# Kernel tuning notes

Hardware: AMD Instinct MI355X
Metric: run time of the kernel (lower is better)

## Reference

```python
import jax, jax.numpy as jnp
import numpy as np

B, T, C = 2, 2048, 2048
H, D = 16, 128


def _rope(x, cos, sin):
    # x: [B,H,T,D], cos/sin: [T,D//2]
    half = x.shape[-1] // 2
    x1, x2 = x[..., :half], x[..., half:]
    c = cos[None, None, :, :]
    s = sin[None, None, :, :]
    return jnp.concatenate([x1 * c - x2 * s, x1 * s + x2 * c], axis=-1)


def setup_inputs() -> dict:
    key = jax.random.key(0)
    k1, k2, k3, k4, k5 = jax.random.split(key, 5)
    x = jax.random.normal(k1, (B, T, C), dtype=jnp.float32)
    cos = jax.random.uniform(k2, (T, D // 2), dtype=jnp.float32)
    sin = jax.random.uniform(k3, (T, D // 2), dtype=jnp.float32)
    scale = 1.0 / np.sqrt(C)
    W_qkv = jax.random.normal(k4, (C, 3 * C), dtype=jnp.float32) * scale
    W_proj = jax.random.normal(k5, (C, C), dtype=jnp.float32) * scale
    return {"x": x, "cos": cos, "sin": sin, "W_qkv": W_qkv, "W_proj": W_proj}


def reference(x, cos, sin, W_qkv, W_proj):
    Bx, Tx, Cx = x.shape
    qkv = x @ W_qkv  # [B,T,3C]
    q, k, v = jnp.split(qkv, 3, axis=-1)
    # [B,T,C] -> [B,H,T,D]
    q = q.reshape(Bx, Tx, H, D).transpose(0, 2, 1, 3)
    k = k.reshape(Bx, Tx, H, D).transpose(0, 2, 1, 3)
    v = v.reshape(Bx, Tx, H, D).transpose(0, 2, 1, 3)
    q = _rope(q, cos, sin)
    k = _rope(k, cos, sin)
    # causal SDPA
    scores = jnp.einsum("bhqd,bhkd->bhqk", q, k) / jnp.sqrt(jnp.float32(D))
    causal = jnp.tril(jnp.ones((Tx, Tx), dtype=bool))
    scores = jnp.where(causal[None, None], scores, jnp.finfo(scores.dtype).min)
    attn = jax.nn.softmax(scores, axis=-1)
    out = jnp.einsum("bhqk,bhkd->bhqd", attn, v)
    out = out.transpose(0, 2, 1, 3).reshape(Bx, Tx, Cx)
    return out @ W_proj
```

## Files before the change

### kernel.cpp

```cpp
#include <hip/hip_runtime.h>
#include <stdint.h>

#define B_  2
#define T_  2048
#define C_  2048
#define H_  16
#define D_  128
#define BH_ 32
#define M_  4096

typedef __attribute__((ext_vector_type(8))) __bf16  bf16x8;
typedef __attribute__((ext_vector_type(4))) float   floatx4;
typedef __attribute__((ext_vector_type(4))) ushort  ushortx4;
typedef __attribute__((ext_vector_type(8))) ushort  ushortx8;

__device__ __forceinline__ ushort f2bf(float f) {
    union { float f; uint32_t u; } v; v.f = f;
    return (ushort)((v.u + 0x7fffu + ((v.u >> 16) & 1u)) >> 16);
}

__device__ __forceinline__ float bf2f(ushort u) {
    union { uint32_t u; float f; } v; v.u = ((uint32_t)u) << 16;
    return v.f;
}

__device__ __forceinline__ floatx4 mfma_bf16(bf16x8 a, bf16x8 b, floatx4 c) {
    return __builtin_amdgcn_mfma_f32_16x16x32_bf16(a, b, c, 0, 0, 0);
}

__device__ __forceinline__ void async16(const ushort* g, ushort* l) {
    __builtin_amdgcn_global_load_lds(
        (const __attribute__((address_space(1))) uint32_t*)g,
        (__attribute__((address_space(3))) uint32_t*)l, 16, 0, 0);
}

__global__ __launch_bounds__(256) void convert_bf16(
    const float* __restrict__ X, ushort* __restrict__ Xb)
{
    const int i = blockIdx.x * 256 + threadIdx.x;
    const float4 v = ((const float4*)X)[i];
    ushortx4 p = { f2bf(v.x), f2bf(v.y), f2bf(v.z), f2bf(v.w) };
    ((ushortx4*)Xb)[i] = p;
}

__global__ __launch_bounds__(256) void transpose_w(
    const float* __restrict__ W, ushort* __restrict__ Wt, int Kdim, int Ndim)
{
    __shared__ float tile[32][33];
    const int n0 = blockIdx.x * 32, k0 = blockIdx.y * 32;
    const int tx = threadIdx.x, ty = threadIdx.y;
    #pragma unroll
    for (int j = 0; j < 4; j++)
        tile[ty + j*8][tx] = W[(size_t)(k0 + ty + j*8) * Ndim + n0 + tx];
    __syncthreads();
    #pragma unroll
    for (int j = 0; j < 4; j++)
        Wt[(size_t)(n0 + ty + j*8) * Kdim + k0 + tx] = f2bf(tile[tx][ty + j*8]);
}

struct FragA { bf16x8 f[4][2]; };
struct FragB { bf16x8 f[2][2]; };

__device__ __forceinline__ void load_a(FragA& fa, const ushort* Ab, int base,
                                       int lr, int quad)
{
    #pragma unroll
    for (int mi2 = 0; mi2 < 4; mi2++)
        #pragma unroll
        for (int kk = 0; kk < 2; kk++) {
            const int row = base + mi2 * 16 + lr;
            fa.f[mi2][kk] = *(const bf16x8*)(
                Ab + row * 64 + (((kk * 4 + quad) ^ (lr & 7)) << 3));
        }
}

__device__ __forceinline__ void load_b(FragB& fb, const ushort* Bb, int base,
                                       int lr, int quad)
{
    #pragma unroll
    for (int ni2 = 0; ni2 < 2; ni2++)
        #pragma unroll
        for (int kk = 0; kk < 2; kk++) {
            const int row = base + ni2 * 16 + lr;
            fb.f[ni2][kk] = *(const bf16x8*)(
                Bb + row * 64 + (((kk * 4 + quad) ^ (lr & 7)) << 3));
        }
}

__device__ __forceinline__ void mfma_quad(floatx4 (&acc)[8][4], const FragA& fa,
                                          const FragB& fb, int mh, int nh)
{
    #pragma unroll
    for (int mi2 = 0; mi2 < 4; mi2++)
        #pragma unroll
        for (int ni2 = 0; ni2 < 2; ni2++)
            #pragma unroll
            for (int kk = 0; kk < 2; kk++)
                acc[mh*4 + mi2][nh*2 + ni2] =
                    mfma_bf16(fa.f[mi2][kk], fb.f[ni2][kk],
                              acc[mh*4 + mi2][nh*2 + ni2]);
}

__device__ __forceinline__ void stage64(const ushort* __restrict__ gsrc,
                                        ushort* ldst, int blk, int k0, int tid)
{
    const int lane = tid & 63;
    const int w8   = tid >> 6;
    const int rl   = lane >> 3;
    const int u    = lane & 7;
    const int row  = (blk << 6) + (w8 << 3) + rl;
    const ushort* g = gsrc + (size_t)row * C_ + k0 + ((u ^ rl) << 3);
    async16(g, ldst + (blk << 12) + (w8 << 9));
}

__device__ __forceinline__ void kloop_8ph(
    const ushort* __restrict__ Ablk, const ushort* __restrict__ Bblk,
    ushort* lds, floatx4 (&acc)[8][4], int tid)
{
    const int lane = tid & 63;
    const int w    = tid >> 6;
    const int wr   = w >> 2;
    const int wc   = w & 3;
    const int lr   = lane & 15;
    const int quad = lane >> 4;

    #pragma unroll
    for (int blk = 0; blk < 4; blk++) {
        stage64(Ablk, lds,         blk, 0, tid);
        stage64(Bblk, lds + 32768, blk, 0, tid);
    }
    #pragma unroll
    for (int blk = 0; blk < 4; blk++) {
        stage64(Ablk, lds + 16384, blk, 64, tid);
        stage64(Bblk, lds + 49152, blk, 64, tid);
    }
    asm volatile("s_waitcnt vmcnt(8)" ::: "memory");
    __builtin_amdgcn_sched_barrier(0);
    __builtin_amdgcn_s_barrier();

    FragA fa0, fa1;
    FragB fb0, fb1;

    #pragma unroll 2
    for (int t = 0; t < 32; ++t) {
        const int p = t & 1;
        ushort* Ab = lds + (p << 14);
        ushort* Bb = lds + 32768 + (p << 14);
        const int k2 = (t + 2) << 6;
        const bool st = (t < 30);

        load_a(fa0, Ab, wr * 128, lr, quad);
        load_b(fb0, Bb, wc * 64, lr, quad);
        __builtin_amdgcn_s_barrier();
        asm volatile("s_waitcnt lgkmcnt(0)" ::: "memory");
        __builtin_amdgcn_sched_barrier(0);
        __builtin_amdgcn_s_setprio(1);
        mfma_quad(acc, fa0, fb0, 0, 0);
        __builtin_amdgcn_s_setprio(0);
        __builtin_amdgcn_s_barrier();

        load_b(fb1, Bb, wc * 64 + 32, lr, quad);
        if (st) { stage64(Ablk, Ab, 0, k2, tid);
                  stage64(Ablk, Ab, 2, k2, tid); }
        __builtin_amdgcn_s_barrier();
        asm volatile("s_waitcnt lgkmcnt(0)" ::: "memory");
        __builtin_amdgcn_sched_barrier(0);
        __builtin_amdgcn_s_setprio(1);
        mfma_quad(acc, fa0, fb1, 0, 1);
        __builtin_amdgcn_s_setprio(0);
        __builtin_amdgcn_s_barrier();

        load_a(fa1, Ab, wr * 128 + 64, lr, quad);
        if (st) { stage64(Bblk, Bb, 0, k2, tid);
                  stage64(Bblk, Bb, 1, k2, tid);
                  stage64(Bblk, Bb, 2, k2, tid); }
        __builtin_amdgcn_s_barrier();
        asm volatile("s_waitcnt lgkmcnt(0)" ::: "memory");
        __builtin_amdgcn_sched_barrier(0);
        __builtin_amdgcn_s_setprio(1);
        mfma_quad(acc, fa1, fb0, 1, 0);
        __builtin_amdgcn_s_setprio(0);
        __builtin_amdgcn_s_barrier();

        if (st) { stage64(Bblk, Bb, 3, k2, tid);
                  stage64(Ablk, Ab, 1, k2, tid);
                  stage64(Ablk, Ab, 3, k2, tid); }
        if (st) asm volatile("s_waitcnt vmcnt(8)" ::: "memory");
        else    asm volatile("s_waitcnt vmcnt(0)" ::: "memory");
        __builtin_amdgcn_sched_barrier(0);
        __builtin_amdgcn_s_barrier();
        __builtin_amdgcn_s_setprio(1);
        mfma_quad(acc, fa1, fb1, 1, 1);
        __builtin_amdgcn_s_setprio(0);
        __builtin_amdgcn_s_barrier();
    }
}

__global__ __launch_bounds__(512, 2) void gemm_bt_8ph(
    const ushort* __restrict__ A, const ushort* __restrict__ Bt,
    float* __restrict__ Co)
{
    __shared__ __align__(16) ushort lds[65536];

    const int tid  = threadIdx.x;
    const int lane = tid & 63;
    const int w    = tid >> 6;
    const int wr   = w >> 2;
    const int wc   = w & 3;
    const int lr   = lane & 15;
    const int quad = lane >> 4;

    int bid = (int)blockIdx.x;
    bid = (bid & 7) * 16 + (bid >> 3);
    const int bx = bid & 7;
    const int by = bid >> 3;

    const ushort* Ablk = A  + (size_t)(by * 256) * C_;
    const ushort* Bblk = Bt + (size_t)(bx * 256) * C_;

    floatx4 acc[8][4];
    #pragma unroll
    for (int i = 0; i < 8; i++)
        #pragma unroll
        for (int j = 0; j < 4; j++)
            acc[i][j] = (floatx4){0.f, 0.f, 0.f, 0.f};

    kloop_8ph(Ablk, Bblk, lds, acc, tid);

    const size_t row0 = (size_t)by * 256 + wr * 128;
    const size_t col0 = (size_t)bx * 256 + wc * 64;
    #pragma unroll
    for (int mi = 0; mi < 8; mi++)
        #pragma unroll
        for (int ni = 0; ni < 4; ni++)
            #pragma unroll
            for (int r = 0; r < 4; r++)
                Co[(row0 + mi*16 + quad*4 + r) * (size_t)C_ + col0 + ni*16 + lr]
                    = acc[mi][ni][r];
}

__global__ __launch_bounds__(512, 2) void gemm_qkv_8ph(
    const ushort* __restrict__ A, const ushort* __restrict__ Bt,
    const float* __restrict__ cosb, const float* __restrict__ sinb,
    ushort* __restrict__ qb, ushort* __restrict__ kbf, ushort* __restrict__ vt)
{
    __shared__ __align__(16) ushort lds[65536];

    const int tid  = threadIdx.x;
    const int lane = tid & 63;
    const int w    = tid >> 6;
    const int wr   = w >> 2;
    const int wc   = w & 3;
    const int lr   = lane & 15;
    const int quad = lane >> 4;

    int bid = (int)blockIdx.x;
    bid = (bid & 7) * 48 + (bid >> 3);
    const int bx = bid % 24;
    const int by = bid / 24;

    const ushort* Ablk = A  + (size_t)(by * 256) * C_;
    const ushort* Bblk = Bt + (size_t)(bx * 256) * C_;

    floatx4 acc[8][4];
    #pragma unroll
    for (int i = 0; i < 8; i++)
        #pragma unroll
        for (int j = 0; j < 4; j++)
            acc[i][j] = (floatx4){0.f, 0.f, 0.f, 0.f};

    kloop_8ph(Ablk, Bblk, lds, acc, tid);

    const int qt  = bx >> 3;
    const int h0  = (bx & 7) << 1;
    const int b   = by >> 3;
    const int t0g = (by & 7) << 8;

    __syncthreads();

    if (qt < 2) {
        #pragma unroll
        for (int mi = 0; mi < 8; mi++)
            #pragma unroll
            for (int ni = 0; ni < 4; ni++)
                #pragma unroll
                for (int r = 0; r < 4; r++) {
                    const int tt = wr * 128 + mi * 16 + quad * 4 + r;
                    const int cc = wc * 64 + ni * 16 + lr;
                    lds[tt * 256 + ((((cc >> 3) ^ (tt & 31)) << 3) | (cc & 7))]
                        = f2bf(acc[mi][ni][r]);
                }
        __syncthreads();

        const int trow = tid >> 1;
        const int hsel = tid & 1;
        const int tg   = t0g + trow;
        const int bh   = b * 16 + h0 + hsel;
        ushort* outp = (qt == 0 ? qb : kbf) + ((size_t)bh * T_ + tg) * D_;
        const float4* cp4 = (const float4*)(cosb + (size_t)tg * 64);
        const float4* sp4 = (const float4*)(sinb + (size_t)tg * 64);
        const ushort* rowp = lds + trow * 256;
        const int tw = trow & 31;
        #pragma unroll
        for (int u = 0; u < 8; u++) {
            bf16x8 x1 = *(const bf16x8*)(rowp + (((hsel * 16 + u)     ^ tw) << 3));
            bf16x8 x2 = *(const bf16x8*)(rowp + (((hsel * 16 + 8 + u) ^ tw) << 3));
            float cc[8], ss[8];
            *(float4*)(cc)     = cp4[u * 2];
            *(float4*)(cc + 4) = cp4[u * 2 + 1];
            *(float4*)(ss)     = sp4[u * 2];
            *(float4*)(ss + 4) = sp4[u * 2 + 1];
            ushortx8 lo, hi;
            #pragma unroll
            for (int e = 0; e < 8; e++) {
                const float x1f = (float)x1[e];
                const float x2f = (float)x2[e];
                lo[e] = f2bf(x1f * cc[e] - x2f * ss[e]);
                hi[e] = f2bf(x1f * ss[e] + x2f * cc[e]);
            }
            *(ushortx8*)(outp + u * 8)      = lo;
            *(ushortx8*)(outp + 64 + u * 8) = hi;
        }
    } else {
        #pragma unroll
        for (int mi = 0; mi < 8; mi++)
            #pragma unroll
            for (int ni = 0; ni < 4; ni++)
                #pragma unroll
                for (int r = 0; r < 4; r++) {
                    const int tt = wr * 128 + mi * 16 + quad * 4 + r;
                    const int cc = wc * 64 + ni * 16 + lr;
                    lds[cc * 256 + ((((tt >> 3) ^ (cc & 31)) << 3) | (tt & 7))]
                        = f2bf(acc[mi][ni][r]);
                }
        __syncthreads();

        const int c  = tid >> 1;
        const int hT = tid & 1;
        const int hh = c >> 7;
        const int d  = c & 127;
        const int bh = b * 16 + h0 + hh;
        const ushort* rowp = lds + c * 256;
        const int cw = c & 31;
        ushort* outp = vt + ((size_t)bh * D_ + d) * T_ + t0g + hT * 128;
        #pragma unroll
        for (int u = 0; u < 16; u++) {
            bf16x8 vv = *(const bf16x8*)(rowp + (((hT * 16 + u) ^ cw) << 3));
            *(bf16x8*)(outp + u * 8) = vv;
        }
    }
}

__global__ __launch_bounds__(256, 4) void flash_attn(
    const ushort* __restrict__ qb, const ushort* __restrict__ kb,
    const ushort* __restrict__ vt, ushort* __restrict__ attnoutb)
{
    __shared__ __align__(16) ushort kt_s[64 * 128];
    __shared__ __align__(16) ushort vt_s[128 * 64];
    __shared__ __align__(16) ushort pl_s[4][16 * 40];

    const int w    = threadIdx.x >> 6;
    const int lane = threadIdx.x & 63;
    const int lr   = lane & 15;
    const int quad = lane >> 4;

    const int bh = blockIdx.x & 31;
    const int m  = 31 - (blockIdx.x >> 5);
    const int qt = 4 * m + w;
    const int qbase = qt * 16;
    const int nk = m + 1;
    const int bb = bh >> 4, hh = bh & 15;

    const ushort* kbp = kb + (size_t)bh * T_ * D_;
    const ushort* vbp = vt + (size_t)bh * D_ * T_;
    ushort* pl = pl_s[w];

    bf16x8 qf[4];
    const ushort* qrow = qb + ((size_t)bh * T_ + qbase + lr) * D_ + quad * 8;
    #pragma unroll
    for (int kc = 0; kc < 4; kc++)
        qf[kc] = *(const bf16x8*)(qrow + kc * 32);

    floatx4 o[8];
    #pragma unroll
    for (int dc = 0; dc < 8; dc++) o[dc] = (floatx4){0.f, 0.f, 0.f, 0.f};
    floatx4 lac = (floatx4){0.f, 0.f, 0.f, 0.f};

    const __bf16 one = (__bf16)1.0f;
    const bf16x8 ones = {one, one, one, one, one, one, one, one};
    const float SCL  = 0.08838834764831845f * 1.4426950408889634f;
    const float BIAS = 23.083120654223414f;

    const int krow4 = lane >> 4;
    const int kunit = lane & 15;
    const int vrow8 = lane >> 3;
    const int vunit = lane & 7;

    for (int kt = 0; kt < nk; ++kt) {
        const int kb0 = kt * 64;
        __syncthreads();
        #pragma unroll
        for (int j = 0; j < 4; j++) {
            const int row = w * 16 + j * 4 + krow4;
            const ushort* gp = kbp + (size_t)(kb0 + row) * D_
                                   + ((kunit ^ (row & 15)) << 3);
            async16(gp, kt_s + (w * 16 + j * 4) * 128);
        }
        #pragma unroll
        for (int j = 0; j < 4; j++) {
            const int row = w * 32 + j * 8 + vrow8;
            const ushort* gp = vbp + (size_t)row * T_ + kb0
                                   + ((vunit ^ (row & 7)) << 3);
            async16(gp, vt_s + (w * 32 + j * 8) * 64);
        }
        __syncthreads();

        #pragma unroll
        for (int half = 0; half < 2; ++half) {
            floatx4 st[2];
            #pragma unroll
            for (int jj = 0; jj < 2; ++jj) {
                const int j = half * 2 + jj;
                floatx4 s = (floatx4){0.f, 0.f, 0.f, 0.f};
                const int kl = j * 16 + lr;
                #pragma unroll
                for (int kc = 0; kc < 4; kc++) {
                    bf16x8 af = *(const bf16x8*)(
                        kt_s + kl * 128 + ((((kc << 2) | quad) ^ lr) << 3));
                    s = mfma_bf16(af, qf[kc], s);
                }
                st[jj] = s;
            }
            #pragma unroll
            for (int jj = 0; jj < 2; ++jj) {
                const int j = half * 2 + jj;
                const int kg0 = kb0 + j * 16 + quad * 4;
                float p[4];
                #pragma unroll
                for (int r = 0; r < 4; r++) {
                    float e = __builtin_amdgcn_exp2f(fmaf(st[jj][r], SCL, -BIAS));
                    p[r] = (kg0 + r > qbase + lr) ? 0.f : e;
                }
                uint2 pk;
                pk.x = (uint32_t)f2bf(p[0]) | ((uint32_t)f2bf(p[1]) << 16);
                pk.y = (uint32_t)f2bf(p[2]) | ((uint32_t)f2bf(p[3]) << 16);
                *(uint2*)(pl + lr * 40 + jj * 16 + quad * 4) = pk;
            }
            bf16x8 pf = *(const bf16x8*)(pl + lr * 40 + quad * 8);
            lac = mfma_bf16(pf, ones, lac);
            #pragma unroll
            for (int dc = 0; dc < 8; dc++) {
                const int d = dc * 16 + lr;
                bf16x8 vf = *(const bf16x8*)(
                    vt_s + d * 64 + ((((half << 2) | quad) ^ (lr & 7)) << 3));
                o[dc] = mfma_bf16(pf, vf, o[dc]);
            }
        }
    }

    #pragma unroll
    for (int dc = 0; dc < 8; dc++)
        #pragma unroll
        for (int r = 0; r < 4; r++) {
            const int trow = qbase + quad * 4 + r;
            attnoutb[((size_t)(bb * T_ + trow)) * C_ + hh * D_ + dc * 16 + lr]
                = f2bf(o[dc][r] / lac[r]);
        }
}

extern "C" void kernel_launch(void* const* d_in, const int* in_sizes, int n_in,
                              void* d_out, int out_size, void* d_ws, size_t ws_size,
                              hipStream_t stream)
{
    (void)in_sizes; (void)n_in; (void)out_size; (void)ws_size;
    const float* x     = (const float*)d_in[0];
    const float* cosb  = (const float*)d_in[1];
    const float* sinb  = (const float*)d_in[2];
    const float* Wqkv  = (const float*)d_in[3];
    const float* Wproj = (const float*)d_in[4];
    float* out = (float*)d_out;

    char* ws = (char*)d_ws;
    ushort* xb       = (ushort*)(ws);
    ushort* Wtq      = (ushort*)(ws + 16777216);
    ushort* Wtp      = (ushort*)(ws + 41943040);
    ushort* qb       = (ushort*)(ws + 50331648);
    ushort* kbf      = (ushort*)(ws + 67108864);
    ushort* vt       = (ushort*)(ws + 83886080);
    ushort* attnoutb = (ushort*)(ws + 100663296);

    dim3 tb32(32, 8);
    transpose_w<<<dim3(3 * C_ / 32, C_ / 32), tb32, 0, stream>>>(Wqkv, Wtq, C_, 3 * C_);
    transpose_w<<<dim3(C_ / 32, C_ / 32),     tb32, 0, stream>>>(Wproj, Wtp, C_, C_);
    convert_bf16<<<(M_ * C_ / 4) / 256, 256, 0, stream>>>(x, xb);

    gemm_qkv_8ph<<<384, 512, 0, stream>>>(xb, Wtq, cosb, sinb, qb, kbf, vt);

    flash_attn<<<BH_ * 32, 256, 0, stream>>>(qb, kbf, vt, attnoutb);

    gemm_bt_8ph<<<128, 512, 0, stream>>>(attnoutb, Wtp, out);
}
```

Before: 412.7 us.

## Replace 8-phase interleaved GEMM k-loop with simpler per-iteration staging schedule

Removes the 8-phase schedule that interleaved global-to-LDS staging with MFMA quads and used barriers between phases. The new loop loads fragments and runs all four MFMA quads with no intermediate barriers, reuses one A fragment register set, then issues all eight staging loads for tile t+2 at the end of the iteration behind a single barrier. This cuts barrier count and register pressure, but global loads are no longer spread across the compute phases, which may reduce overlap of memory and MFMA work.

Result: no change. 416.6 us (+0.9%).

```diff
diff --git a/kernel.cpp b/kernel.cpp
--- a/kernel.cpp
+++ b/kernel.cpp
@@ -113,7 +113,7 @@
     async16(g, ldst + (blk << 12) + (w8 << 9));
 }
 
-__device__ __forceinline__ void kloop_8ph(
+__device__ __forceinline__ void kloop(
     const ushort* __restrict__ Ablk, const ushort* __restrict__ Bblk,
     ushort* lds, floatx4 (&acc)[8][4], int tid)
 {
@@ -138,9 +138,6 @@
     __builtin_amdgcn_sched_barrier(0);
     __builtin_amdgcn_s_barrier();
 
-    FragA fa0, fa1;
-    FragB fb0, fb1;
-
     #pragma unroll 2
     for (int t = 0; t < 32; ++t) {
         const int p = t & 1;
@@ -149,49 +146,47 @@
         const int k2 = (t + 2) << 6;
         const bool st = (t < 30);
 
-        load_a(fa0, Ab, wr * 128, lr, quad);
+        FragA fa;
+        FragB fb0, fb1;
+
+        load_a(fa, Ab, wr * 128, lr, quad);
         load_b(fb0, Bb, wc * 64, lr, quad);
-        __builtin_amdgcn_s_barrier();
         asm volatile("s_waitcnt lgkmcnt(0)" ::: "memory");
         __builtin_amdgcn_sched_barrier(0);
         __builtin_amdgcn_s_setprio(1);
-        mfma_quad(acc, fa0, fb0, 0, 0);
+        mfma_quad(acc, fa, fb0, 0, 0);
         __builtin_amdgcn_s_setprio(0);
-        __builtin_amdgcn_s_barrier();
 
         load_b(fb1, Bb, wc * 64 + 32, lr, quad);
-        if (st) { stage64(Ablk, Ab, 0, k2, tid);
-                  stage64(Ablk, Ab, 2, k2, tid); }
-        __builtin_amdgcn_s_barrier();
         asm volatile("s_waitcnt lgkmcnt(0)" ::: "memory");
         __builtin_amdgcn_sched_barrier(0);
         __builtin_amdgcn_s_setprio(1);
-        mfma_quad(acc, fa0, fb1, 0, 1);
+        mfma_quad(acc, fa, fb1, 0, 1);
         __builtin_amdgcn_s_setprio(0);
-        __builtin_amdgcn_s_barrier();
-
-        load_a(fa1, Ab, wr * 128 + 64, lr, quad);
-        if (st) { stage64(Bblk, Bb, 0, k2, tid);
-                  stage64(Bblk, Bb, 1, k2, tid);
-                  stage64(Bblk, Bb, 2, k2, tid); }
-        __builtin_amdgcn_s_barrier();
+
+        load_a(fa, Ab, wr * 128 + 64, lr, quad);
         asm volatile("s_waitcnt lgkmcnt(0)" ::: "memory");
         __builtin_amdgcn_sched_barrier(0);
         __builtin_amdgcn_s_setprio(1);
-        mfma_quad(acc, fa1, fb0, 1, 0);
+        mfma_quad(acc, fa, fb0, 1, 0);
+        mfma_quad(acc, fa, fb1, 1, 1);
         __builtin_amdgcn_s_setprio(0);
+
         __builtin_amdgcn_s_barrier();
-
-        if (st) { stage64(Bblk, Bb, 3, k2, tid);
-                  stage64(Ablk, Ab, 1, k2, tid);
-                  stage64(Ablk, Ab, 3, k2, tid); }
-        if (st) asm volatile("s_waitcnt vmcnt(8)" ::: "memory");
-        else    asm volatile("s_waitcnt vmcnt(0)" ::: "memory");
+        if (st) {
+            stage64(Ablk, Ab, 0, k2, tid);
+            stage64(Ablk, Ab, 1, k2, tid);
+            stage64(Ablk, Ab, 2, k2, tid);
+            stage64(Ablk, Ab, 3, k2, tid);
+            stage64(Bblk, Bb, 0, k2, tid);
+            stage64(Bblk, Bb, 1, k2, tid);
+            stage64(Bblk, Bb, 2, k2, tid);
+            stage64(Bblk, Bb, 3, k2, tid);
+            asm volatile("s_waitcnt vmcnt(8)" ::: "memory");
+        } else {
+            asm volatile("s_waitcnt vmcnt(0)" ::: "memory");
+        }
         __builtin_amdgcn_sched_barrier(0);
-        __builtin_amdgcn_s_barrier();
-        __builtin_amdgcn_s_setprio(1);
-        mfma_quad(acc, fa1, fb1, 1, 1);
-        __builtin_amdgcn_s_setprio(0);
         __builtin_amdgcn_s_barrier();
     }
 }
@@ -225,7 +220,7 @@
         for (int j = 0; j < 4; j++)
             acc[i][j] = (floatx4){0.f, 0.f, 0.f, 0.f};
 
-    kloop_8ph(Ablk, Bblk, lds, acc, tid);
+    kloop(Ablk, Bblk, lds, acc, tid);
 
     const size_t row0 = (size_t)by * 256 + wr * 128;
     const size_t col0 = (size_t)bx * 256 + wc * 64;
@@ -269,7 +264,7 @@
         for (int j = 0; j < 4; j++)
             acc[i][j] = (floatx4){0.f, 0.f, 0.f, 0.f};
 
-    kloop_8ph(Ablk, Bblk, lds, acc, tid);
+    kloop(Ablk, Bblk, lds, acc, tid);
 
     const int qt  = bx >> 3;
     const int h0  = (bx & 7) << 1;
```
